# Kernel tuning notes

Measured on AMD Instinct MI355X. Metric: run time of the kernel, lower is better.

The kernel has to match this reference:

```python
import jax, jax.numpy as jnp
import numpy as np

LAMDA = 0.5
TEMPERATURE = 0.07
EPS = 1e-5


def setup_inputs() -> dict:
    key = jax.random.key(0)
    k1, k2, k3 = jax.random.split(key, 3)
    N, D = 8192, 128
    features = jax.random.normal(k1, (N, D), dtype=jnp.float32)
    labels = jax.random.randint(k2, (N,), 0, 100, dtype=jnp.int64 if jax.config.jax_enable_x64 else jnp.int32)
    domain_labels = jax.random.randint(k3, (N,), 0, 4, dtype=jnp.int64 if jax.config.jax_enable_x64 else jnp.int32)
    return {"features": features, "labels": labels, "domain_labels": domain_labels}


def reference(features, labels, domain_labels):
    N = features.shape[0]
    # L2-normalize rows (torch.nn.functional.normalize, eps=1e-12)
    norms = jnp.maximum(jnp.linalg.norm(features, axis=1, keepdims=True), 1e-12)
    f = features / norms
    sim = jnp.matmul(f, f.T) / TEMPERATURE  # [N, N]

    same_label = labels[:, None] == labels[None, :]
    same_dom = domain_labels[:, None] == domain_labels[None, :]
    offdiag = ~jnp.eye(N, dtype=bool)

    # per-pair domain weight: lamda in-domain, (1-lamda) out-of-domain
    w_exp = jnp.where(same_dom, LAMDA, 1.0 - LAMDA) * jnp.exp(sim)

    # denominator: all off-diagonal pairs (positives + negatives), weighted
    denom = jnp.sum(jnp.where(offdiag, w_exp, 0.0), axis=1) + EPS  # [N]

    pos = same_label & offdiag
    log_frac = jnp.log(w_exp / denom[:, None] + EPS)
    num_pos = jnp.sum(pos, axis=1)  # [N]
    loss_i = jnp.sum(jnp.where(pos, log_frac, 0.0), axis=1) / jnp.maximum(num_pos, 1)

    # anchors with zero positives produce NaN in torch and are skipped
    valid = num_pos > 0
    nans = jnp.sum(~valid)
    loss = -jnp.sum(jnp.where(valid, loss_i, 0.0))
    return loss / (N - nans + 1)
```

## Files before the change

### kernel.cpp

```cpp
#include <hip/hip_runtime.h>

#define NROWS 8192
#define DDIM  128
#define NBLK  (NROWS / 128)
#define NLAB  100
#define GCAP  160
#define GNJT  (GCAP / 16)
#define EPSV  1e-5f
#define LN2F  0.69314718055994530942f
#define FSCALE 4.53981643f

typedef short s16x8 __attribute__((ext_vector_type(8)));
typedef float f32x4 __attribute__((ext_vector_type(4)));
typedef unsigned short u16;
typedef unsigned int u32;

__device__ __forceinline__ u16 f2bf(float x) {
  u32 b = __builtin_bit_cast(u32, x);
  u32 r = (b + 0x7FFFu + ((b >> 16) & 1u)) >> 16;
  return (u16)r;
}

__global__ __launch_bounds__(256) void zero_kernel(float* __restrict__ denom) {
  denom[blockIdx.x * 256 + threadIdx.x] = 0.0f;
}

__global__ __launch_bounds__(256) void norm_kernel(
    const float* __restrict__ feat, u16* __restrict__ g) {
  int wave = threadIdx.x >> 6;
  int lane = threadIdx.x & 63;
  int row = (blockIdx.x << 2) + wave;
  const float* fr = feat + (size_t)row * DDIM + (lane << 1);
  float2 v = *(const float2*)fr;
  float ss = v.x * v.x + v.y * v.y;
#pragma unroll
  for (int m = 1; m < 64; m <<= 1) ss += __shfl_xor(ss, m);
  float inv = FSCALE / fmaxf(sqrtf(ss), 1e-12f);
  ushort2 o;
  o.x = f2bf(v.x * inv);
  o.y = f2bf(v.y * inv);
  *(ushort2*)(g + (size_t)row * DDIM + (lane << 1)) = o;
}

__global__ __launch_bounds__(256) void bucket_kernel(
    const int* __restrict__ lab, int* __restrict__ offs,
    int* __restrict__ cnts, int* __restrict__ rowlist) {
  __shared__ int h[NLAB], cur[NLAB], off[NLAB];
  int tid = threadIdx.x;
  if (tid < NLAB) h[tid] = 0;
  __syncthreads();
  for (int i = tid; i < NROWS; i += 256) atomicAdd(&h[lab[i]], 1);
  __syncthreads();
  if (tid == 0) {
    int s = 0;
    for (int l = 0; l < NLAB; ++l) { off[l] = s; s += h[l]; }
  }
  __syncthreads();
  if (tid < NLAB) { cur[tid] = off[tid]; offs[tid] = off[tid]; cnts[tid] = h[tid]; }
  __syncthreads();
  for (int i = tid; i < NROWS; i += 256) {
    int p = atomicAdd(&cur[lab[i]], 1);
    rowlist[p] = i;
  }
}

#define LOADB_TO(bv, BsArr, jt)                                              \
  _Pragma("unroll")                                                          \
  for (int kc = 0; kc < 4; ++kc) {                                           \
    const int c_ = (kc << 2) + lh;                                           \
    bv[kc] = *(const s16x8*)(&BsArr[(size_t)((jt)*16 + lr) * DDIM +          \
                                    ((c_ ^ (lr & 7)) << 3)]);                \
  }

#define MFMA_TO(accv, bv, init0, init1)                                      \
  accv[0] = init0; accv[1] = init1;                                          \
  __builtin_amdgcn_s_setprio(1);                                             \
  _Pragma("unroll")                                                          \
  for (int kc = 0; kc < 4; ++kc) {                                           \
    accv[0] = __builtin_amdgcn_mfma_f32_16x16x32_bf16(a[0][kc], bv[kc],      \
                                                      accv[0], 0, 0, 0);     \
    accv[1] = __builtin_amdgcn_mfma_f32_16x16x32_bf16(a[1][kc], bv[kc],      \
                                                      accv[1], 0, 0, 0);     \
  }                                                                          \
  __builtin_amdgcn_s_setprio(0);

#define EPI_T(accv, jt)                                                      \
  {                                                                          \
    const int tj0 = j0 + (jt)*16;                                            \
    float csum = 0.f;                                                        \
    if (diagblk) {                                                           \
      _Pragma("unroll")                                                      \
      for (int rf = 0; rf < 2; ++rf)                                         \
      _Pragma("unroll")                                                      \
        for (int r = 0; r < 4; ++r) {                                        \
          float e_ = __builtin_amdgcn_exp2f(accv[rf][r]);                    \
          e_ = (gibase[rf] + r == tj0 + lr) ? 0.0f : e_;                     \
          dacc[rf][r] += e_;                                                 \
        }                                                                    \
    } else {                                                                 \
      _Pragma("unroll")                                                      \
      for (int rf = 0; rf < 2; ++rf)                                         \
      _Pragma("unroll")                                                      \
        for (int r = 0; r < 4; ++r) {                                        \
          float e_ = __builtin_amdgcn_exp2f(accv[rf][r]);                    \
          dacc[rf][r] += e_;                                                 \
          csum += e_;                                                        \
        }                                                                    \
      csum += __shfl_xor(csum, 16);                                          \
      csum += __shfl_xor(csum, 32);                                          \
      ccol[jt] = csum;                                                       \
    }                                                                        \
  }

__global__ __launch_bounds__(256, 4) void denom_tri(
    const u16* __restrict__ g, float* __restrict__ denom) {
  const int bi = blockIdx.x, bj = blockIdx.y;
  if (bj < bi) return;
  __shared__ u16 Bs[128 * DDIM];
  const int tid = threadIdx.x;
  const int wave = tid >> 6, lane = tid & 63;
  const int lr = lane & 15, lh = lane >> 4;
  const int i0 = bi * 128 + wave * 32;
  const int j0 = bj * 128;
  const bool diagblk = (bi == bj);

  {
    const int cs = (tid & 15) ^ ((tid >> 4) & 7);
#pragma unroll
    for (int k = 0; k < 8; ++k) {
      const u16* src = g + (size_t)(j0 + k * 16 + (tid >> 4)) * DDIM + (cs << 3);
      u16* dst = &Bs[(size_t)(k * 16 + (wave << 2)) * DDIM];
      __builtin_amdgcn_global_load_lds(
          (const __attribute__((address_space(1))) void*)src,
          (__attribute__((address_space(3))) void*)dst, 16, 0, 0);
    }
  }

  s16x8 a[2][4];
#pragma unroll
  for (int rf = 0; rf < 2; ++rf) {
    const u16* gr = g + (size_t)(i0 + rf * 16 + lr) * DDIM + lh * 8;
#pragma unroll
    for (int kc = 0; kc < 4; ++kc) a[rf][kc] = *(const s16x8*)(gr + kc * 32);
  }
  const int gibase[2] = {i0 + lh * 4, i0 + 16 + lh * 4};

  asm volatile("s_waitcnt vmcnt(0)" ::: "memory");
  __builtin_amdgcn_s_barrier();

  float dacc[2][4] = {};
  float ccol[8] = {};
  const f32x4 m1 = f32x4{-1.f, -1.f, -1.f, -1.f};

  s16x8 b0[4], b1[4];
  f32x4 acc0[2], acc1[2];

  LOADB_TO(b0, Bs, 0)
  MFMA_TO(acc0, b0, m1, m1)
#pragma unroll
  for (int p = 0; p < 3; ++p) {
    LOADB_TO(b1, Bs, 2 * p + 1)
    MFMA_TO(acc1, b1, m1, m1)
    EPI_T(acc0, 2 * p)
    LOADB_TO(b0, Bs, 2 * p + 2)
    MFMA_TO(acc0, b0, m1, m1)
    EPI_T(acc1, 2 * p + 1)
  }
  LOADB_TO(b1, Bs, 7)
  MFMA_TO(acc1, b1, m1, m1)
  EPI_T(acc0, 6)
  EPI_T(acc1, 7)

#pragma unroll
  for (int rf = 0; rf < 2; ++rf)
#pragma unroll
    for (int r = 0; r < 4; ++r) {
      float v = dacc[rf][r];
      v += __shfl_xor(v, 1); v += __shfl_xor(v, 2);
      v += __shfl_xor(v, 4); v += __shfl_xor(v, 8);
      if (lr == 0) atomicAdd(&denom[gibase[rf] + r], v);
    }
  if (!diagblk) {
#pragma unroll
    for (int jt = 0; jt < 8; ++jt)
      if (lane < 16) atomicAdd(&denom[j0 + jt * 16 + lane], ccol[jt]);
  }
}

__global__ __launch_bounds__(320) void group_loss(
    const u16* __restrict__ g, const int* __restrict__ offs,
    const int* __restrict__ cnts, const int* __restrict__ rowlist,
    const float* __restrict__ denom,
    float* __restrict__ rowloss, int* __restrict__ rowvalid) {
  __shared__ u16 Bs[GCAP * DDIM];
  const int lb = blockIdx.x;
  const int cnt = cnts[lb];
  if (cnt == 0) return;
  const int off = offs[lb];
  const int tid = threadIdx.x;
  const int wave = tid >> 6, lane = tid & 63;
  const int lr = lane & 15, lh = lane >> 4;

#pragma unroll
  for (int s = 0; s < 8; ++s) {
    const int m = s * 320 + tid;
    const int rloc = m >> 4, cc = m & 15;
    const int cs = cc ^ (rloc & 7);
    const int grow = rowlist[off + (rloc < cnt ? rloc : 0)];
    const u16* src = g + (size_t)grow * DDIM + (cs << 3);
    u16* dst = &Bs[(size_t)(s * 320 + wave * 64) * 8];
    __builtin_amdgcn_global_load_lds(
        (const __attribute__((address_space(1))) void*)src,
        (__attribute__((address_space(3))) void*)dst, 16, 0, 0);
  }

  s16x8 a[2][4];
#pragma unroll
  for (int rf = 0; rf < 2; ++rf) {
    const int ar = wave * 32 + rf * 16 + lr;
    const int gar = rowlist[off + (ar < cnt ? ar : 0)];
    const u16* gr = g + (size_t)gar * DDIM + lh * 8;
#pragma unroll
    for (int kc = 0; kc < 4; ++kc) a[rf][kc] = *(const s16x8*)(gr + kc * 32);
  }
  const int erow[2] = {wave * 32 + lh * 4, wave * 32 + 16 + lh * 4};
  f32x4 cinit[2];
#pragma unroll
  for (int rf = 0; rf < 2; ++rf)
#pragma unroll
    for (int r = 0; r < 4; ++r) {
      const int er = erow[rf] + r;
      const int gi = rowlist[off + (er < cnt ? er : 0)];
      cinit[rf][r] = -__builtin_amdgcn_logf(denom[gi] + EPSV) - 1.0f;
    }

  asm volatile("s_waitcnt vmcnt(0)" ::: "memory");
  __builtin_amdgcn_s_barrier();

  float lacc[2][4] = {};

#pragma unroll
  for (int jt = 0; jt < GNJT; ++jt) {
    s16x8 b[4];
    LOADB_TO(b, Bs, jt)
    f32x4 acc[2];
    MFMA_TO(acc, b, cinit[0], cinit[1])
    const int col = jt * 16 + lr;
    const bool colok = (col < cnt);
#pragma unroll
    for (int rf = 0; rf < 2; ++rf)
#pragma unroll
      for (int r = 0; r < 4; ++r) {
        const int er = erow[rf] + r;
        const bool valid = colok && (er < cnt) && (er != col);
        float x = __builtin_amdgcn_exp2f(acc[rf][r]) + EPSV;
        float lf = __builtin_amdgcn_logf(x);
        lacc[rf][r] += valid ? lf : 0.0f;
      }
  }

#pragma unroll
  for (int rf = 0; rf < 2; ++rf)
#pragma unroll
    for (int r = 0; r < 4; ++r) {
      float v = lacc[rf][r];
      v += __shfl_xor(v, 1); v += __shfl_xor(v, 2);
      v += __shfl_xor(v, 4); v += __shfl_xor(v, 8);
      const int er = erow[rf] + r;
      if (lr == 0 && er < cnt) {
        const int i = rowlist[off + er];
        const int np = cnt - 1;
        rowvalid[i] = (np > 0) ? 1 : 0;
        rowloss[i] = (np > 0) ? (v * LN2F / (float)np) : 0.0f;
      }
    }
}

__global__ __launch_bounds__(256) void final_reduce(
    const float* __restrict__ rowloss, const int* __restrict__ rowvalid,
    float* __restrict__ out) {
  __shared__ float sL[256];
  __shared__ int sV[256];
  int tid = threadIdx.x;
  float a = 0.f;
  int v = 0;
  for (int i = tid; i < NROWS; i += 256) {
    a += rowloss[i];
    v += rowvalid[i];
  }
  sL[tid] = a; sV[tid] = v;
  __syncthreads();
  for (int s = 128; s > 0; s >>= 1) {
    if (tid < s) { sL[tid] += sL[tid + s]; sV[tid] += sV[tid + s]; }
    __syncthreads();
  }
  if (tid == 0) {
    out[0] = -sL[0] / (float)(sV[0] + 1);
  }
}

extern "C" void kernel_launch(void* const* d_in, const int* in_sizes, int n_in,
                              void* d_out, int out_size, void* d_ws, size_t ws_size,
                              hipStream_t stream) {
  const float* feat = (const float*)d_in[0];
  const int* labels = (const int*)d_in[1];
  float* out = (float*)d_out;

  char* ws = (char*)d_ws;
  u16* g        = (u16*)(ws);
  float* denom  = (float*)(ws + (2u << 20));
  int* offs     = (int*)(ws + (2u << 20) + 32768);
  int* cnts     = (int*)(ws + (2u << 20) + 33280);
  int* rowlist  = (int*)(ws + (2u << 20) + 65536);
  float* rowloss= (float*)(ws + (2u << 20) + 131072);
  int* rowvalid = (int*)(ws + (2u << 20) + 163840);

  zero_kernel<<<NROWS / 256, 256, 0, stream>>>(denom);
  norm_kernel<<<NROWS / 4, 256, 0, stream>>>(feat, g);
  bucket_kernel<<<1, 256, 0, stream>>>(labels, offs, cnts, rowlist);
  denom_tri<<<dim3(NBLK, NBLK), 256, 0, stream>>>(g, denom);
  group_loss<<<NLAB, 320, 0, stream>>>(g, offs, cnts, rowlist, denom, rowloss, rowvalid);
  final_reduce<<<1, 256, 0, stream>>>(rowloss, rowvalid, out);
}
```

Measured before the change: 73.46 us.

## Launch only upper-triangle blocks, fuse histogram into norm, reduce loss with atomics

The denominator kernel now launches a linear grid holding only the upper-triangle block pairs and recovers (bi, bj) with a sqrt-based index, so half the launched blocks no longer exit immediately. The label histogram and the denom zeroing move into the normalisation kernel through global atomics, and the scatter kernel runs with 1024 threads. Per-row loss arrays and the 8192-element final reduction are replaced by per-wave atomic accumulation into a scalar, plus a tiny final kernel that counts valid rows from the label counts. This trims launch and memory overhead in the small kernels, at the cost of global atomic contention on the histogram and nondeterministic float summation order.

```diff
diff --git a/kernel.cpp b/kernel.cpp
--- a/kernel.cpp
+++ b/kernel.cpp
@@ -3,6 +3,7 @@
 #define NROWS 8192
 #define DDIM  128
 #define NBLK  (NROWS / 128)
+#define NTRI  (NBLK * (NBLK + 1) / 2)
 #define NLAB  100
 #define GCAP  160
 #define GNJT  (GCAP / 16)
@@ -21,12 +22,16 @@
   return (u16)r;
 }
 
-__global__ __launch_bounds__(256) void zero_kernel(float* __restrict__ denom) {
-  denom[blockIdx.x * 256 + threadIdx.x] = 0.0f;
+__global__ __launch_bounds__(256) void init_kernel(
+    int* __restrict__ cnt, float* __restrict__ Lsum) {
+  int t = threadIdx.x;
+  if (t < 128) cnt[t] = 0;
+  if (t == 128) *Lsum = 0.0f;
 }
 
 __global__ __launch_bounds__(256) void norm_kernel(
-    const float* __restrict__ feat, u16* __restrict__ g) {
+    const float* __restrict__ feat, const int* __restrict__ lab,
+    u16* __restrict__ g, int* __restrict__ cnt, float* __restrict__ denom) {
   int wave = threadIdx.x >> 6;
   int lane = threadIdx.x & 63;
   int row = (blockIdx.x << 2) + wave;
@@ -40,25 +45,25 @@
   o.x = f2bf(v.x * inv);
   o.y = f2bf(v.y * inv);
   *(ushort2*)(g + (size_t)row * DDIM + (lane << 1)) = o;
-}
-
-__global__ __launch_bounds__(256) void bucket_kernel(
-    const int* __restrict__ lab, int* __restrict__ offs,
-    int* __restrict__ cnts, int* __restrict__ rowlist) {
-  __shared__ int h[NLAB], cur[NLAB], off[NLAB];
+  if (lane == 0) {
+    atomicAdd(&cnt[lab[row]], 1);
+    denom[row] = 0.0f;
+  }
+}
+
+__global__ __launch_bounds__(1024) void scatter_kernel(
+    const int* __restrict__ lab, const int* __restrict__ cnt,
+    int* __restrict__ offs, int* __restrict__ rowlist) {
+  __shared__ int off[NLAB], cur[NLAB];
   int tid = threadIdx.x;
-  if (tid < NLAB) h[tid] = 0;
-  __syncthreads();
-  for (int i = tid; i < NROWS; i += 256) atomicAdd(&h[lab[i]], 1);
-  __syncthreads();
   if (tid == 0) {
     int s = 0;
-    for (int l = 0; l < NLAB; ++l) { off[l] = s; s += h[l]; }
+    for (int l = 0; l < NLAB; ++l) { off[l] = s; s += cnt[l]; }
   }
   __syncthreads();
-  if (tid < NLAB) { cur[tid] = off[tid]; offs[tid] = off[tid]; cnts[tid] = h[tid]; }
+  if (tid < NLAB) { cur[tid] = off[tid]; offs[tid] = off[tid]; }
   __syncthreads();
-  for (int i = tid; i < NROWS; i += 256) {
+  for (int i = tid; i < NROWS; i += 1024) {
     int p = atomicAdd(&cur[lab[i]], 1);
     rowlist[p] = i;
   }
@@ -114,8 +119,13 @@
 
 __global__ __launch_bounds__(256, 4) void denom_tri(
     const u16* __restrict__ g, float* __restrict__ denom) {
-  const int bi = blockIdx.x, bj = blockIdx.y;
-  if (bj < bi) return;
+  const int lin = blockIdx.x;
+  int bi = (int)(64.5 - sqrt(4160.25 - 2.0 * (double)lin));
+  if (bi < 0) bi = 0;
+  while ((bi + 1) * NBLK - (bi + 1) * bi / 2 <= lin) ++bi;
+  while (bi * NBLK - bi * (bi - 1) / 2 > lin) --bi;
+  const int bj = bi + (lin - (bi * NBLK - bi * (bi - 1) / 2));
+
   __shared__ u16 Bs[128 * DDIM];
   const int tid = threadIdx.x;
   const int wave = tid >> 6, lane = tid & 63;
@@ -190,12 +200,11 @@
 __global__ __launch_bounds__(320) void group_loss(
     const u16* __restrict__ g, const int* __restrict__ offs,
     const int* __restrict__ cnts, const int* __restrict__ rowlist,
-    const float* __restrict__ denom,
-    float* __restrict__ rowloss, int* __restrict__ rowvalid) {
+    const float* __restrict__ denom, float* __restrict__ Lsum) {
   __shared__ u16 Bs[GCAP * DDIM];
   const int lb = blockIdx.x;
   const int cnt = cnts[lb];
-  if (cnt == 0) return;
+  if (cnt < 2) return;
   const int off = offs[lb];
   const int tid = threadIdx.x;
   const int wave = tid >> 6, lane = tid & 63;
@@ -259,6 +268,8 @@
       }
   }
 
+  const float scale = LN2F / (float)(cnt - 1);
+  float wtot = 0.f;
 #pragma unroll
   for (int rf = 0; rf < 2; ++rf)
 #pragma unroll
@@ -267,36 +278,25 @@
       v += __shfl_xor(v, 1); v += __shfl_xor(v, 2);
       v += __shfl_xor(v, 4); v += __shfl_xor(v, 8);
       const int er = erow[rf] + r;
-      if (lr == 0 && er < cnt) {
-        const int i = rowlist[off + er];
-        const int np = cnt - 1;
-        rowvalid[i] = (np > 0) ? 1 : 0;
-        rowloss[i] = (np > 0) ? (v * LN2F / (float)np) : 0.0f;
-      }
+      if (lr == 0 && er < cnt) wtot += v * scale;
     }
-}
-
-__global__ __launch_bounds__(256) void final_reduce(
-    const float* __restrict__ rowloss, const int* __restrict__ rowvalid,
+  wtot += __shfl_xor(wtot, 1);  wtot += __shfl_xor(wtot, 2);
+  wtot += __shfl_xor(wtot, 4);  wtot += __shfl_xor(wtot, 8);
+  wtot += __shfl_xor(wtot, 16); wtot += __shfl_xor(wtot, 32);
+  if (lane == 0 && wtot != 0.0f) atomicAdd(Lsum, wtot);
+}
+
+__global__ __launch_bounds__(64) void final_kernel(
+    const int* __restrict__ cnts, const float* __restrict__ Lsum,
     float* __restrict__ out) {
-  __shared__ float sL[256];
-  __shared__ int sV[256];
-  int tid = threadIdx.x;
-  float a = 0.f;
+  int lane = threadIdx.x;
   int v = 0;
-  for (int i = tid; i < NROWS; i += 256) {
-    a += rowloss[i];
-    v += rowvalid[i];
-  }
-  sL[tid] = a; sV[tid] = v;
-  __syncthreads();
-  for (int s = 128; s > 0; s >>= 1) {
-    if (tid < s) { sL[tid] += sL[tid + s]; sV[tid] += sV[tid + s]; }
-    __syncthreads();
-  }
-  if (tid == 0) {
-    out[0] = -sL[0] / (float)(sV[0] + 1);
-  }
+  if (lane < NLAB) { int c = cnts[lane]; v += (c > 1) ? c : 0; }
+  if (lane + 64 < NLAB) { int c = cnts[lane + 64]; v += (c > 1) ? c : 0; }
+  v += __shfl_xor(v, 1);  v += __shfl_xor(v, 2);
+  v += __shfl_xor(v, 4);  v += __shfl_xor(v, 8);
+  v += __shfl_xor(v, 16); v += __shfl_xor(v, 32);
+  if (lane == 0) out[0] = -Lsum[0] / (float)(v + 1);
 }
 
 extern "C" void kernel_launch(void* const* d_in, const int* in_sizes, int n_in,
@@ -309,16 +309,15 @@
   char* ws = (char*)d_ws;
   u16* g        = (u16*)(ws);
   float* denom  = (float*)(ws + (2u << 20));
-  int* offs     = (int*)(ws + (2u << 20) + 32768);
-  int* cnts     = (int*)(ws + (2u << 20) + 33280);
+  int* cnt      = (int*)(ws + (2u << 20) + 32768);
+  int* offs     = (int*)(ws + (2u << 20) + 33280);
+  float* Lsum   = (float*)(ws + (2u << 20) + 33792);
   int* rowlist  = (int*)(ws + (2u << 20) + 65536);
-  float* rowloss= (float*)(ws + (2u << 20) + 131072);
-  int* rowvalid = (int*)(ws + (2u << 20) + 163840);
-
-  zero_kernel<<<NROWS / 256, 256, 0, stream>>>(denom);
-  norm_kernel<<<NROWS / 4, 256, 0, stream>>>(feat, g);
-  bucket_kernel<<<1, 256, 0, stream>>>(labels, offs, cnts, rowlist);
-  denom_tri<<<dim3(NBLK, NBLK), 256, 0, stream>>>(g, denom);
-  group_loss<<<NLAB, 320, 0, stream>>>(g, offs, cnts, rowlist, denom, rowloss, rowvalid);
-  final_reduce<<<1, 256, 0, stream>>>(rowloss, rowvalid, out);
-}
+
+  init_kernel<<<1, 256, 0, stream>>>(cnt, Lsum);
+  norm_kernel<<<NROWS / 4, 256, 0, stream>>>(feat, labels, g, cnt, denom);
+  scatter_kernel<<<1, 1024, 0, stream>>>(labels, cnt, offs, rowlist);
+  denom_tri<<<NTRI, 256, 0, stream>>>(g, denom);
+  group_loss<<<NLAB, 320, 0, stream>>>(g, offs, cnt, rowlist, denom, Lsum);
+  final_kernel<<<1, 64, 0, stream>>>(cnt, Lsum, out);
+}
```

After: 81.55 us. 1.11x slower.
